# Kernel optimization log

Measured on AMD Instinct MI355X. Metric: run time of the kernel, lower is better.

The kernel has to match this reference:

```python
import jax, jax.numpy as jnp
import numpy as np

BATCH, SEQ, D_IN, D_STATE = 8, 4096, 1024, 64


def setup_inputs() -> dict:
    key = jax.random.key(0)
    ks = jax.random.split(key, 3)
    u = jax.random.normal(ks[0], (BATCH, SEQ, D_IN), dtype=jnp.float32)
    log_A = jnp.zeros((D_STATE,), dtype=jnp.float32)
    B = jax.random.normal(ks[1], (D_STATE, D_IN), dtype=jnp.float32) * 0.01
    C = jax.random.normal(ks[2], (D_IN, D_STATE), dtype=jnp.float32) * 0.01
    D = jnp.ones((D_IN,), dtype=jnp.float32)
    log_delta = jnp.zeros((D_IN,), dtype=jnp.float32)
    return {"u": u, "log_A": log_A, "B": B, "C": C, "D": D, "log_delta": log_delta}


def reference(u, log_A, B, C, D, log_delta):
    batch, seq_len, input_dim = u.shape
    state_dim = log_A.shape[0]
    delta = jax.nn.softplus(log_delta)                      # [I]
    A = -jnp.exp(log_A)                                     # [N]
    A_bar = jnp.exp(delta[:, None] * A[None, :])            # [I, N]
    A_bar_state = A_bar.mean(axis=0)                        # [N]
    B_bar = B * delta[None, :]                              # [N, I]
    # Precompute input projections for all timesteps: [B, T, N]
    Bu = jnp.einsum('ni,bti->btn', B_bar, u)
    x0 = jnp.zeros((batch, state_dim), dtype=u.dtype)

    def step(x, bu_t):
        x = x * A_bar_state[None, :] + bu_t
        return x, x

    _, xs = jax.lax.scan(step, x0, jnp.swapaxes(Bu, 0, 1))  # xs: [T, B, N]
    xs = jnp.swapaxes(xs, 0, 1)                             # [B, T, N]
    y = jnp.einsum('in,btn->bti', C, xs) + D[None, None, :] * u
    return y
```

## Files before the change

kernel.cpp:

```cpp
#include <hip/hip_runtime.h>
#include <cstdint>

#define BATCH 8
#define SEQ   4096
#define DIN   1024
#define DST   64
#define CHUNK 32
#define NCC   (SEQ/CHUNK)
#define NBLK1 (BATCH*NCC)

typedef __attribute__((ext_vector_type(8))) short short8;
typedef __attribute__((ext_vector_type(4))) short short4v;
typedef __attribute__((ext_vector_type(4))) float f32x4;

__device__ __forceinline__ short f2bf(float f) {
    union { float f; unsigned u; } v; v.f = f;
    unsigned r = v.u + 0x7fffu + ((v.u >> 16) & 1u);
    return (short)(r >> 16);
}
__device__ __forceinline__ float softplus_f(float x) {
    return (x > 20.f) ? x : log1pf(expf(x));
}

__global__ void ssm_k0(const float* __restrict__ logA, const float* __restrict__ Bm,
                       const float* __restrict__ Cm, const float* __restrict__ logdelta,
                       short* __restrict__ Bb, short* __restrict__ Cb,
                       float* __restrict__ a_o, float* __restrict__ l2a_o,
                       float* __restrict__ aL_o)
{
    __shared__ float red[256];
    int blk = blockIdx.x, tid = threadIdx.x;
    if (blk < DST) {
        int n = blk;
        float An = -expf(logA[n]);
        float acc = 0.f;
        #pragma unroll
        for (int ii = 0; ii < DIN/256; ++ii) {
            int i = ii*256 + tid;
            float dlt = softplus_f(logdelta[i]);
            Bb[n*DIN + i] = f2bf(Bm[n*DIN + i] * dlt);
            acc += expf(dlt * An);
        }
        red[tid] = acc; __syncthreads();
        for (int s = 128; s > 0; s >>= 1) {
            if (tid < s) red[tid] += red[tid + s];
            __syncthreads();
        }
        if (tid == 0) {
            float a = red[0] * (1.f/DIN);
            a_o[n]   = a;
            l2a_o[n] = log2f(a);
            float p = a;
            #pragma unroll
            for (int q = 0; q < 5; ++q) p = p*p;
            aL_o[n] = p;
        }
    } else {
        int base = (blk - DST) * (DIN*DST/16);
        for (int e = tid; e < DIN*DST/16; e += 256)
            Cb[base + e] = f2bf(Cm[base + e]);
    }
}

__global__ __launch_bounds__(256) void ssm_k1(
    const float* __restrict__ u, const short* __restrict__ Bb,
    const float* __restrict__ a_i, float* __restrict__ xloc, float* __restrict__ carry)
{
    int blk = blockIdx.x;
    int b = blk >> 7, cc = blk & (NCC-1);
    int tid = threadIdx.x;
    int w = tid >> 6, lane = tid & 63;
    int wr = w & 1, wk = w >> 1;
    int m = lane & 15, quad = lane >> 4;

    long row = ((long)b << 12) + (cc << 5) + (wr << 4) + m;
    const float* up  = u  + row * DIN + wk*(DIN/2) + quad * 8;
    const short* bb0 = Bb + wk*(DIN/2) + quad * 8;

    f32x4 acc0 = {0,0,0,0}, acc1 = {0,0,0,0}, acc2 = {0,0,0,0}, acc3 = {0,0,0,0};

    #pragma unroll 4
    for (int ks = 0; ks < DIN/64; ++ks) {
        const float4* uv = (const float4*)(up + ks*32);
        float4 ua = uv[0];
        float4 ub = uv[1];
        short8 af;
        af[0]=f2bf(ua.x); af[1]=f2bf(ua.y); af[2]=f2bf(ua.z); af[3]=f2bf(ua.w);
        af[4]=f2bf(ub.x); af[5]=f2bf(ub.y); af[6]=f2bf(ub.z); af[7]=f2bf(ub.w);
        const short* bbase = bb0 + ks*32;
        short8 b0 = *(const short8*)(bbase + ( 0 + m)*DIN);
        short8 b1 = *(const short8*)(bbase + (16 + m)*DIN);
        short8 b2 = *(const short8*)(bbase + (32 + m)*DIN);
        short8 b3 = *(const short8*)(bbase + (48 + m)*DIN);
        acc0 = __builtin_amdgcn_mfma_f32_16x16x32_bf16(af, b0, acc0, 0,0,0);
        acc1 = __builtin_amdgcn_mfma_f32_16x16x32_bf16(af, b1, acc1, 0,0,0);
        acc2 = __builtin_amdgcn_mfma_f32_16x16x32_bf16(af, b2, acc2, 0,0,0);
        acc3 = __builtin_amdgcn_mfma_f32_16x16x32_bf16(af, b3, acc3, 0,0,0);
    }

    __shared__ float bu[2][CHUNK][DST+1];
    int trow = (wr << 4) + (quad << 2);
    #pragma unroll
    for (int r = 0; r < 4; ++r) {
        bu[wk][trow + r][ 0 + m] = acc0[r];
        bu[wk][trow + r][16 + m] = acc1[r];
        bu[wk][trow + r][32 + m] = acc2[r];
        bu[wk][trow + r][48 + m] = acc3[r];
    }
    __syncthreads();

    if (tid < DST) {
        int n = tid;
        float an = a_i[n];
        float x = 0.f;
        float* xp = xloc + (((long)b << 12) + (cc << 5)) * DST + n;
        #pragma unroll
        for (int t = 0; t < CHUNK; ++t) {
            x = x * an + (bu[0][t][n] + bu[1][t][n]);
            xp[(long)t * DST] = x;
        }
        carry[blk * DST + n] = x;
    }
}

__global__ __launch_bounds__(256) void ssm_k3(
    const float* __restrict__ u, const float* __restrict__ xloc,
    const float* __restrict__ carry, const float* __restrict__ aLp,
    const float* __restrict__ l2a, const short* __restrict__ Cb,
    const float* __restrict__ Dv, float* __restrict__ y)
{
    int tblk = blockIdx.x;
    long t0 = (long)tblk << 4;
    int b = (int)(t0 >> 12);
    int tloc0 = (int)(t0 & (SEQ-1));
    int c = tloc0 >> 5;
    int jbase = tloc0 & (CHUNK-1);

    __shared__ float E_lds[DST];
    __shared__ short xs[16][72];

    int tid = threadIdx.x;
    if (tid < DST) {
        int n = tid;
        float al = aLp[n];
        float E = 0.f;
        const float* cp = carry + (b*NCC)*DST + n;
        #pragma unroll 4
        for (int p = 0; p < c; ++p)
            E = E * al + cp[p*DST];
        E_lds[n] = E;
    }
    __syncthreads();

    {
        int m  = tid >> 4;
        int n0 = (tid & 15) * 4;
        long t = t0 + m;
        int j  = jbase + m;
        float4 xv = *(const float4*)(xloc + t*DST + n0);
        float4 la = *(const float4*)(l2a + n0);
        float4 Ev = *(const float4*)(&E_lds[n0]);
        float jp = (float)(j + 1);
        short4v xsv;
        xsv[0] = f2bf(xv.x + exp2f(jp*la.x)*Ev.x);
        xsv[1] = f2bf(xv.y + exp2f(jp*la.y)*Ev.y);
        xsv[2] = f2bf(xv.z + exp2f(jp*la.z)*Ev.z);
        xsv[3] = f2bf(xv.w + exp2f(jp*la.w)*Ev.w);
        *(short4v*)(&xs[m][n0]) = xsv;
    }
    __syncthreads();

    int w = tid >> 6, lane = tid & 63;
    int l16 = lane & 15, quad = lane >> 4;

    short8 x0 = *(const short8*)(&xs[l16][ 0 + quad*8]);
    short8 x1 = *(const short8*)(&xs[l16][32 + quad*8]);

    long trow = t0 + l16;
    const float* urow = u + trow*DIN;
    float* yrow = y + trow*DIN;

    #pragma unroll 4
    for (int ii = 0; ii < 16; ++ii) {
        int i0 = (ii*4 + w) * 16;
        const short* cb = Cb + (long)(i0 + l16)*DST + quad*8;
        short8 c0 = *(const short8*)(cb);
        short8 c1 = *(const short8*)(cb + 32);
        f32x4 acc = {0,0,0,0};
        acc = __builtin_amdgcn_mfma_f32_16x16x32_bf16(c0, x0, acc, 0,0,0);
        acc = __builtin_amdgcn_mfma_f32_16x16x32_bf16(c1, x1, acc, 0,0,0);
        int ib = i0 + (quad << 2);
        float4 dd = *(const float4*)(Dv + ib);
        float4 uu = *(const float4*)(urow + ib);
        float4 o;
        o.x = acc[0] + dd.x*uu.x;
        o.y = acc[1] + dd.y*uu.y;
        o.z = acc[2] + dd.z*uu.z;
        o.w = acc[3] + dd.w*uu.w;
        *(float4*)(yrow + ib) = o;
    }
}

extern "C" void kernel_launch(void* const* d_in, const int* in_sizes, int n_in,
                              void* d_out, int out_size, void* d_ws, size_t ws_size,
                              hipStream_t stream)
{
    const float* u        = (const float*)d_in[0];
    const float* logA     = (const float*)d_in[1];
    const float* Bm       = (const float*)d_in[2];
    const float* Cm       = (const float*)d_in[3];
    const float* D        = (const float*)d_in[4];
    const float* logdelta = (const float*)d_in[5];
    float* y = (float*)d_out;

    char* ws = (char*)d_ws;
    float* xloc  = (float*)(ws);
    float* carry = (float*)(ws + 8u*1024*1024);
    short* Bb    = (short*)(ws + 8u*1024*1024 + 256*1024);
    short* Cb    = (short*)(ws + 8u*1024*1024 + 384*1024);
    float* a_o   = (float*)(ws + 8u*1024*1024 + 512*1024);
    float* l2a_o = a_o + 64;
    float* aL_o  = a_o + 128;

    hipLaunchKernelGGL(ssm_k0, dim3(DST + 16), dim3(256), 0, stream,
                       logA, Bm, Cm, logdelta, Bb, Cb, a_o, l2a_o, aL_o);
    hipLaunchKernelGGL(ssm_k1, dim3(NBLK1), dim3(256), 0, stream,
                       u, Bb, a_o, xloc, carry);
    hipLaunchKernelGGL(ssm_k3, dim3((BATCH*SEQ)/16), dim3(256), 0, stream,
                       u, xloc, carry, aL_o, l2a_o, Cb, D, y);
}
```

Before: 318.2 us.

## Add parallel carry-scan kernel, stage u through LDS, coalesce y output

Adds a separate kernel that runs a Hillis-Steele parallel prefix scan over the chunk carries. Each output tile then loads its starting state directly, instead of running a serial recurrence over up to 127 carries per block. The input-projection kernel now loads u into LDS with coalesced float4 reads and converts it to bf16 there, and the warps split the output across state columns instead of across K halves. The output kernel stages MFMA results in LDS so the y stores and u reads are row-contiguous. In exchange it adds one kernel launch, more LDS use and extra barriers.

```diff
diff --git a/kernel.cpp b/kernel.cpp
--- a/kernel.cpp
+++ b/kernel.cpp
@@ -70,42 +70,47 @@
     int b = blk >> 7, cc = blk & (NCC-1);
     int tid = threadIdx.x;
     int w = tid >> 6, lane = tid & 63;
-    int wr = w & 1, wk = w >> 1;
-    int m = lane & 15, quad = lane >> 4;
-
-    long row = ((long)b << 12) + (cc << 5) + (wr << 4) + m;
-    const float* up  = u  + row * DIN + wk*(DIN/2) + quad * 8;
-    const short* bb0 = Bb + wk*(DIN/2) + quad * 8;
-
-    f32x4 acc0 = {0,0,0,0}, acc1 = {0,0,0,0}, acc2 = {0,0,0,0}, acc3 = {0,0,0,0};
-
-    #pragma unroll 4
-    for (int ks = 0; ks < DIN/64; ++ks) {
-        const float4* uv = (const float4*)(up + ks*32);
-        float4 ua = uv[0];
-        float4 ub = uv[1];
-        short8 af;
-        af[0]=f2bf(ua.x); af[1]=f2bf(ua.y); af[2]=f2bf(ua.z); af[3]=f2bf(ua.w);
-        af[4]=f2bf(ub.x); af[5]=f2bf(ub.y); af[6]=f2bf(ub.z); af[7]=f2bf(ub.w);
-        const short* bbase = bb0 + ks*32;
-        short8 b0 = *(const short8*)(bbase + ( 0 + m)*DIN);
-        short8 b1 = *(const short8*)(bbase + (16 + m)*DIN);
-        short8 b2 = *(const short8*)(bbase + (32 + m)*DIN);
-        short8 b3 = *(const short8*)(bbase + (48 + m)*DIN);
-        acc0 = __builtin_amdgcn_mfma_f32_16x16x32_bf16(af, b0, acc0, 0,0,0);
-        acc1 = __builtin_amdgcn_mfma_f32_16x16x32_bf16(af, b1, acc1, 0,0,0);
-        acc2 = __builtin_amdgcn_mfma_f32_16x16x32_bf16(af, b2, acc2, 0,0,0);
-        acc3 = __builtin_amdgcn_mfma_f32_16x16x32_bf16(af, b3, acc3, 0,0,0);
-    }
-
-    __shared__ float bu[2][CHUNK][DST+1];
-    int trow = (wr << 4) + (quad << 2);
-    #pragma unroll
-    for (int r = 0; r < 4; ++r) {
-        bu[wk][trow + r][ 0 + m] = acc0[r];
-        bu[wk][trow + r][16 + m] = acc1[r];
-        bu[wk][trow + r][32 + m] = acc2[r];
-        bu[wk][trow + r][48 + m] = acc3[r];
+    int wm = w & 1, wn = w >> 1;
+    int l16 = lane & 15, quad = lane >> 4;
+
+    __shared__ short us[CHUNK][520];
+    __shared__ float bu[CHUNK][DST+1];
+
+    long rowbase = ((long)b << 12) + (cc << 5);
+    f32x4 acc0 = {0,0,0,0}, acc1 = {0,0,0,0};
+
+    for (int s2 = 0; s2 < 2; ++s2) {
+        #pragma unroll
+        for (int it = 0; it < 16; ++it) {
+            int f = it*256 + tid;
+            int row = f >> 7;
+            int c4  = f & 127;
+            float4 v = *(const float4*)(u + (rowbase + row)*DIN + s2*512 + c4*4);
+            short4v sv;
+            sv[0]=f2bf(v.x); sv[1]=f2bf(v.y); sv[2]=f2bf(v.z); sv[3]=f2bf(v.w);
+            *(short4v*)(&us[row][c4*4]) = sv;
+        }
+        __syncthreads();
+        const short* bbn0 = Bb + (wn*32 +  0 + l16)*DIN + s2*512 + quad*8;
+        const short* bbn1 = Bb + (wn*32 + 16 + l16)*DIN + s2*512 + quad*8;
+        #pragma unroll 4
+        for (int ks = 0; ks < 16; ++ks) {
+            short8 af = *(const short8*)(&us[wm*16 + l16][ks*32 + quad*8]);
+            short8 b0 = *(const short8*)(bbn0 + ks*32);
+            short8 b1 = *(const short8*)(bbn1 + ks*32);
+            acc0 = __builtin_amdgcn_mfma_f32_16x16x32_bf16(af, b0, acc0, 0,0,0);
+            acc1 = __builtin_amdgcn_mfma_f32_16x16x32_bf16(af, b1, acc1, 0,0,0);
+        }
+        __syncthreads();
+    }
+
+    {
+        int trow = wm*16 + (quad << 2);
+        #pragma unroll
+        for (int r = 0; r < 4; ++r) {
+            bu[trow + r][wn*32 +  0 + l16] = acc0[r];
+            bu[trow + r][wn*32 + 16 + l16] = acc1[r];
+        }
     }
     __syncthreads();
 
@@ -113,21 +118,53 @@
         int n = tid;
         float an = a_i[n];
         float x = 0.f;
-        float* xp = xloc + (((long)b << 12) + (cc << 5)) * DST + n;
+        float* xp = xloc + rowbase * DST + n;
         #pragma unroll
         for (int t = 0; t < CHUNK; ++t) {
-            x = x * an + (bu[0][t][n] + bu[1][t][n]);
+            x = x * an + bu[t][n];
             xp[(long)t * DST] = x;
         }
         carry[blk * DST + n] = x;
+    }
+}
+
+__global__ __launch_bounds__(256) void ssm_k2(
+    const float* __restrict__ carry, const float* __restrict__ aLp,
+    float* __restrict__ Xin)
+{
+    __shared__ float v[2][NCC][DST+1];
+    int b = blockIdx.x, tid = threadIdx.x;
+    int n = tid & 63;
+    for (int f = tid; f < NCC*DST; f += 256) {
+        int c = f >> 6, nn = f & 63;
+        v[0][c][nn] = carry[(b*NCC + c)*DST + nn];
+    }
+    float fd = aLp[n];
+    __syncthreads();
+    int pp = 0;
+    for (int d = 1; d < NCC; d <<= 1) {
+        #pragma unroll 4
+        for (int r = 0; r < NCC/4; ++r) {
+            int c = (tid >> 6) + r*4;
+            float val = v[pp][c][n];
+            if (c >= d) val += fd * v[pp][c-d][n];
+            v[pp^1][c][n] = val;
+        }
+        fd *= fd;
+        pp ^= 1;
+        __syncthreads();
+    }
+    for (int f = tid; f < NCC*DST; f += 256) {
+        int c = f >> 6, nn = f & 63;
+        Xin[(b*NCC + c)*DST + nn] = (c == 0) ? 0.f : v[pp][c-1][nn];
     }
 }
 
 __global__ __launch_bounds__(256) void ssm_k3(
     const float* __restrict__ u, const float* __restrict__ xloc,
-    const float* __restrict__ carry, const float* __restrict__ aLp,
-    const float* __restrict__ l2a, const short* __restrict__ Cb,
-    const float* __restrict__ Dv, float* __restrict__ y)
+    const float* __restrict__ Xin, const float* __restrict__ l2a,
+    const short* __restrict__ Cb, const float* __restrict__ Dv,
+    float* __restrict__ y)
 {
     int tblk = blockIdx.x;
     long t0 = (long)tblk << 4;
@@ -138,18 +175,11 @@
 
     __shared__ float E_lds[DST];
     __shared__ short xs[16][72];
+    __shared__ float ybuf[16][260];
 
     int tid = threadIdx.x;
-    if (tid < DST) {
-        int n = tid;
-        float al = aLp[n];
-        float E = 0.f;
-        const float* cp = carry + (b*NCC)*DST + n;
-        #pragma unroll 4
-        for (int p = 0; p < c; ++p)
-            E = E * al + cp[p*DST];
-        E_lds[n] = E;
-    }
+    if (tid < DST)
+        E_lds[tid] = Xin[(b*NCC + c)*DST + tid];
     __syncthreads();
 
     {
@@ -176,28 +206,37 @@
     short8 x0 = *(const short8*)(&xs[l16][ 0 + quad*8]);
     short8 x1 = *(const short8*)(&xs[l16][32 + quad*8]);
 
-    long trow = t0 + l16;
-    const float* urow = u + trow*DIN;
-    float* yrow = y + trow*DIN;
-
-    #pragma unroll 4
-    for (int ii = 0; ii < 16; ++ii) {
-        int i0 = (ii*4 + w) * 16;
-        const short* cb = Cb + (long)(i0 + l16)*DST + quad*8;
-        short8 c0 = *(const short8*)(cb);
-        short8 c1 = *(const short8*)(cb + 32);
-        f32x4 acc = {0,0,0,0};
-        acc = __builtin_amdgcn_mfma_f32_16x16x32_bf16(c0, x0, acc, 0,0,0);
-        acc = __builtin_amdgcn_mfma_f32_16x16x32_bf16(c1, x1, acc, 0,0,0);
-        int ib = i0 + (quad << 2);
-        float4 dd = *(const float4*)(Dv + ib);
-        float4 uu = *(const float4*)(urow + ib);
-        float4 o;
-        o.x = acc[0] + dd.x*uu.x;
-        o.y = acc[1] + dd.y*uu.y;
-        o.z = acc[2] + dd.z*uu.z;
-        o.w = acc[3] + dd.w*uu.w;
-        *(float4*)(yrow + ib) = o;
+    for (int s = 0; s < 4; ++s) {
+        #pragma unroll
+        for (int ii = 0; ii < 4; ++ii) {
+            int i0 = s*256 + w*64 + ii*16;
+            const short* cb = Cb + (long)(i0 + l16)*DST + quad*8;
+            short8 c0 = *(const short8*)(cb);
+            short8 c1 = *(const short8*)(cb + 32);
+            f32x4 acc = {0,0,0,0};
+            acc = __builtin_amdgcn_mfma_f32_16x16x32_bf16(c0, x0, acc, 0,0,0);
+            acc = __builtin_amdgcn_mfma_f32_16x16x32_bf16(c1, x1, acc, 0,0,0);
+            *(f32x4*)(&ybuf[l16][w*64 + ii*16 + (quad << 2)]) = acc;
+        }
+        __syncthreads();
+        #pragma unroll
+        for (int k = 0; k < 4; ++k) {
+            int f4 = k*256 + tid;
+            int row = f4 >> 6, c4 = f4 & 63;
+            int col = c4 * 4;
+            int gcol = s*256 + col;
+            long t = t0 + row;
+            float4 yv = *(const float4*)(&ybuf[row][col]);
+            float4 uu = *(const float4*)(u + t*DIN + gcol);
+            float4 dd = *(const float4*)(Dv + gcol);
+            float4 o;
+            o.x = yv.x + dd.x*uu.x;
+            o.y = yv.y + dd.y*uu.y;
+            o.z = yv.z + dd.z*uu.z;
+            o.w = yv.w + dd.w*uu.w;
+            *(float4*)(y + t*DIN + gcol) = o;
+        }
+        __syncthreads();
     }
 }
 
@@ -216,9 +255,10 @@
     char* ws = (char*)d_ws;
     float* xloc  = (float*)(ws);
     float* carry = (float*)(ws + 8u*1024*1024);
-    short* Bb    = (short*)(ws + 8u*1024*1024 + 256*1024);
-    short* Cb    = (short*)(ws + 8u*1024*1024 + 384*1024);
-    float* a_o   = (float*)(ws + 8u*1024*1024 + 512*1024);
+    float* Xin   = (float*)(ws + 8u*1024*1024 + 256*1024);
+    short* Bb    = (short*)(ws + 8u*1024*1024 + 512*1024);
+    short* Cb    = (short*)(ws + 8u*1024*1024 + 640*1024);
+    float* a_o   = (float*)(ws + 8u*1024*1024 + 768*1024);
     float* l2a_o = a_o + 64;
     float* aL_o  = a_o + 128;
 
@@ -226,6 +266,8 @@
                        logA, Bm, Cm, logdelta, Bb, Cb, a_o, l2a_o, aL_o);
     hipLaunchKernelGGL(ssm_k1, dim3(NBLK1), dim3(256), 0, stream,
                        u, Bb, a_o, xloc, carry);
+    hipLaunchKernelGGL(ssm_k2, dim3(BATCH), dim3(256), 0, stream,
+                       carry, aL_o, Xin);
     hipLaunchKernelGGL(ssm_k3, dim3((BATCH*SEQ)/16), dim3(256), 0, stream,
-                       u, xloc, carry, aL_o, l2a_o, Cb, D, y);
-}
+                       u, xloc, Xin, l2a_o, Cb, D, y);
+}
```

New measurement: 342.5 us. 1.08x slower.
